# Kernel tuning notes

Measured on AMD Instinct MI355X. Metric: run time of the kernel, lower is better.

The kernel has to match this reference:

```python
import jax, jax.numpy as jnp
import numpy as np

B, S, D, H = 2, 2048, 1024, 16
HD = D // H


def setup_inputs() -> dict:
    key = jax.random.key(0)
    ks = jax.random.split(key, 9)
    sc = 0.02
    return {
        "x": jax.random.normal(ks[0], (B, S, D), dtype=jnp.float32),
        "qw": jax.random.normal(ks[1], (D, D), dtype=jnp.float32) * sc,
        "qb": jax.random.normal(ks[2], (D,), dtype=jnp.float32) * sc,
        "kw": jax.random.normal(ks[3], (D, D), dtype=jnp.float32) * sc,
        "kb": jax.random.normal(ks[4], (D,), dtype=jnp.float32) * sc,
        "vw": jax.random.normal(ks[5], (D, D), dtype=jnp.float32) * sc,
        "vb": jax.random.normal(ks[6], (D,), dtype=jnp.float32) * sc,
        "ow": jax.random.normal(ks[7], (D, D), dtype=jnp.float32) * sc,
        "ob": jax.random.normal(ks[8], (D,), dtype=jnp.float32) * sc,
    }


def reference(x, qw, qb, kw, kb, vw, vb, ow, ob):
    b, s, d = x.shape
    # projections (torch Linear: x @ W.T + b)
    q = (x @ qw.T + qb).reshape(b, s, H, HD).transpose(0, 2, 1, 3)  # bhsd
    k = (x @ kw.T + kb).reshape(b, s, H, HD).transpose(0, 2, 1, 3)
    v = (x @ vw.T + vb).reshape(b, s, H, HD).transpose(0, 2, 1, 3)
    scale = 1.0 / jnp.sqrt(jnp.float32(HD))
    score = jnp.einsum("bhsd,bhtd->bhst", q, k) * scale  # bhss
    # causal mask: -inf strictly above diagonal
    mask = jnp.triu(jnp.full((s, s), -jnp.inf, dtype=score.dtype), k=1)
    score = jax.nn.softmax(score + mask, axis=-1)
    o = jnp.einsum("bhst,bhtd->bhsd", score, v)
    o = o.transpose(0, 2, 1, 3).reshape(b, s, d)
    return o @ ow.T + ob
```

## Files before the change

kernel.cpp:

```cpp
#include <hip/hip_runtime.h>
#include <hip/hip_bf16.h>
#include <stdint.h>

typedef __bf16 bf16x8 __attribute__((ext_vector_type(8)));
typedef __bf16 bf16x4 __attribute__((ext_vector_type(4)));
typedef float f32x4 __attribute__((ext_vector_type(4)));
typedef unsigned short ushort_t;


__device__ inline ushort_t f2bf(float f) {
  union { float f; uint32_t u; } v; v.f = f;
  uint32_t r = (v.u + 0x7fffu + ((v.u >> 16) & 1u)) >> 16;
  return (ushort_t)r;
}

__device__ inline void gll16(const void* g, void* l) {
  __builtin_amdgcn_global_load_lds((const __attribute__((address_space(1))) void*)g,
                                   (__attribute__((address_space(3))) void*)l, 16, 0, 0);
}

__global__ void cvt_x(const float* __restrict__ in, ushort_t* __restrict__ out) {
  int i = blockIdx.x * blockDim.x + threadIdx.x;
  float4 f = ((const float4*)in)[i];
  union { ushort_t u[4]; uint2 v; } r;
  r.u[0] = f2bf(f.x); r.u[1] = f2bf(f.y); r.u[2] = f2bf(f.z); r.u[3] = f2bf(f.w);
  ((uint2*)out)[i] = r.v;
}
__global__ void cvt_w(const float* __restrict__ a, const float* __restrict__ b,
                      const float* __restrict__ c, const float* __restrict__ d,
                      ushort_t* __restrict__ out) {
  const float* srcs[4] = {a, b, c, d};
  const float* s = srcs[blockIdx.y];
  ushort_t* o = out + (size_t)blockIdx.y * 1048576;
  int i = blockIdx.x * blockDim.x + threadIdx.x;
  float4 f = ((const float4*)s)[i];
  union { ushort_t u[4]; uint2 v; } r;
  r.u[0] = f2bf(f.x); r.u[1] = f2bf(f.y); r.u[2] = f2bf(f.z); r.u[3] = f2bf(f.w);
  ((uint2*)(o))[i] = r.v;
}

__global__ __launch_bounds__(256) void qkv_gemm(
    const ushort_t* __restrict__ xb,
    const ushort_t* __restrict__ qwb, const ushort_t* __restrict__ kwb, const ushort_t* __restrict__ vwb,
    const float* __restrict__ qbias, const float* __restrict__ kbias, const float* __restrict__ vbias,
    ushort_t* __restrict__ qo, ushort_t* __restrict__ ko, ushort_t* __restrict__ vto)
{
  const int z = blockIdx.z;
  const float* bias = (z == 0) ? qbias : (z == 1) ? kbias : vbias;
  const ushort_t* Ap;
  const ushort_t* Bp;
  int m0, n0;
  if (z == 2) {
    Ap = vwb; Bp = xb;
    m0 = blockIdx.x * 128;
    n0 = blockIdx.y * 128;
  } else {
    Ap = xb; Bp = (z == 0) ? qwb : kwb;
    m0 = blockIdx.y * 128;
    n0 = blockIdx.x * 128;
  }

  __shared__ __align__(16) ushort_t As[128 * 64];
  __shared__ __align__(16) ushort_t Bs[128 * 64];

  const int tid = threadIdx.x;
  const int w = tid >> 6;
  const int lane = tid & 63;
  const int ln = lane & 15;
  const int q4 = lane >> 4;
  const int wm = w & 1, wn = w >> 1;

  f32x4 acc[4][4];
  #pragma unroll
  for (int i = 0; i < 4; i++)
    #pragma unroll
    for (int j = 0; j < 4; j++) acc[i][j] = f32x4{0.f, 0.f, 0.f, 0.f};

  for (int k0 = 0; k0 < 1024; k0 += 64) {
    __syncthreads();
    #pragma unroll
    for (int i = 0; i < 4; i++) {
      int c = tid + i * 256;
      int row = c >> 3;
      int cq = (c & 7) ^ (row & 7);
      gll16(&Ap[(size_t)(m0 + row) * 1024 + k0 + cq * 8], &As[c * 8]);
      gll16(&Bp[(size_t)(n0 + row) * 1024 + k0 + cq * 8], &Bs[c * 8]);
    }
    __syncthreads();
    #pragma unroll
    for (int ks = 0; ks < 2; ks++) {
      bf16x8 af[4], bfr[4];
      #pragma unroll
      for (int t = 0; t < 4; t++) {
        int rr = wm * 64 + t * 16 + ln;
        af[t]  = *(const bf16x8*)(&As[rr * 64 + (((ks * 4 + q4) ^ (rr & 7)) * 8)]);
        int rc = wn * 64 + t * 16 + ln;
        bfr[t] = *(const bf16x8*)(&Bs[rc * 64 + (((ks * 4 + q4) ^ (rc & 7)) * 8)]);
      }
      #pragma unroll
      for (int tm = 0; tm < 4; tm++)
        #pragma unroll
        for (int tn = 0; tn < 4; tn++)
          acc[tm][tn] = __builtin_amdgcn_mfma_f32_16x16x32_bf16(af[tm], bfr[tn], acc[tm][tn], 0, 0, 0);
    }
  }

  if (z == 2) {
    #pragma unroll
    for (int tn = 0; tn < 4; tn++) {
      int col = n0 + wn * 64 + tn * 16 + ln;
      int bb = col >> 11, s = col & 2047;
      size_t base = (size_t)bb * 2097152 + s;
      #pragma unroll
      for (int tm = 0; tm < 4; tm++) {
        int prow = m0 + wm * 64 + tm * 16 + q4 * 4;
        #pragma unroll
        for (int r = 0; r < 4; r++) {
          int p = prow + r;
          vto[base + (size_t)p * 2048] = f2bf(acc[tm][tn][r] + bias[p]);
        }
      }
    }
  } else {
    #pragma unroll
    for (int tn = 0; tn < 4; tn++) {
      int col = n0 + wn * 64 + tn * 16 + ln;
      float bv = bias[col];
      int h = col >> 6, hd = col & 63;
      #pragma unroll
      for (int tm = 0; tm < 4; tm++) {
        int rowb = m0 + wm * 64 + tm * 16 + q4 * 4;
        #pragma unroll
        for (int r = 0; r < 4; r++) {
          int row = rowb + r;
          int b = row >> 11, s = row & 2047;
          float val = acc[tm][tn][r] + bv;
          if (z == 0) {
            qo[((size_t)((b * 16 + h) * 2048 + s)) * 64 + hd] = f2bf(val * 0.180336884f);
          } else {
            ko[((size_t)((b * 16 + h) * 2048 + s)) * 64 + hd] = f2bf(val);
          }
        }
      }
    }
  }
}

#define PAD 72
#define PPAD 68
__global__ __launch_bounds__(256) void attn(
    const ushort_t* __restrict__ qp, const ushort_t* __restrict__ kp,
    const ushort_t* __restrict__ vtp, ushort_t* __restrict__ op)
{
  __shared__ __align__(16) ushort_t Ks[64 * PAD];
  __shared__ __align__(16) ushort_t Vts[64 * PAD];
  __shared__ __align__(16) ushort_t Ps[8][16 * PPAD];

  const int tid = threadIdx.x;
  const int w = tid >> 6;
  const int lane = tid & 63;
  const int ln = lane & 15;
  const int q4 = lane >> 4;
  const int bh = blockIdx.y;
  const int b = bh >> 4, h = bh & 15;
  int tswz = (blockIdx.x + blockIdx.y) & 15;
  const int qt = (blockIdx.y & 16) ? (15 - tswz) : tswz;
  const int q0 = qt * 128;
  const int nt = 2 * qt + 2;

  const int c0 = tid, c1 = tid + 256;
  const int kr0_row = c0 >> 3, kr0_col = (c0 & 7) * 8;
  const int kr1_row = c1 >> 3, kr1_col = (c1 & 7) * 8;

  bf16x8 onesf;
  {
    union { ushort_t u[8]; bf16x8 v; } t;
    #pragma unroll
    for (int j = 0; j < 8; j++) t.u[j] = 0x3F80;
    onesf = t.v;
  }

  bf16x8 qf[2][2];
  #pragma unroll
  for (int s = 0; s < 2; s++) {
    const ushort_t* base = qp + ((size_t)bh * 2048 + q0 + w * 32 + s * 16 + ln) * 64 + q4 * 8;
    qf[s][0] = *(const bf16x8*)(base);
    qf[s][1] = *(const bf16x8*)(base + 32);
  }

  f32x4 acc_o[2][4];
  f32x4 acc_l[2];
  #pragma unroll
  for (int s = 0; s < 2; s++) {
    acc_l[s] = f32x4{0.f, 0.f, 0.f, 0.f};
    #pragma unroll
    for (int t = 0; t < 4; t++) acc_o[s][t] = f32x4{0.f, 0.f, 0.f, 0.f};
  }

  uint4 kr0, kr1, vr0, vr1;
  {
    const ushort_t* kb = kp + (size_t)bh * 2048 * 64;
    kr0 = *(const uint4*)(kb + kr0_row * 64 + kr0_col);
    kr1 = *(const uint4*)(kb + kr1_row * 64 + kr1_col);
    const ushort_t* vb = vtp + (size_t)bh * 64 * 2048;
    vr0 = *(const uint4*)(vb + (size_t)kr0_row * 2048 + kr0_col);
    vr1 = *(const uint4*)(vb + (size_t)kr1_row * 2048 + kr1_col);
  }

  for (int it = 0; it < nt; it++) {
    if (it) __syncthreads();
    *(uint4*)(&Ks [kr0_row * PAD + kr0_col]) = kr0;
    *(uint4*)(&Ks [kr1_row * PAD + kr1_col]) = kr1;
    *(uint4*)(&Vts[kr0_row * PAD + kr0_col]) = vr0;
    *(uint4*)(&Vts[kr1_row * PAD + kr1_col]) = vr1;
    __syncthreads();

    if (it + 1 < nt) {
      int kv1 = (it + 1) * 64;
      const ushort_t* kb = kp + ((size_t)bh * 2048 + kv1) * 64;
      kr0 = *(const uint4*)(kb + kr0_row * 64 + kr0_col);
      kr1 = *(const uint4*)(kb + kr1_row * 64 + kr1_col);
      const ushort_t* vb = vtp + (size_t)bh * 64 * 2048;
      vr0 = *(const uint4*)(vb + (size_t)kr0_row * 2048 + kv1 + kr0_col);
      vr1 = *(const uint4*)(vb + (size_t)kr1_row * 2048 + kv1 + kr1_col);
    }

    f32x4 sc[2][4];
    #pragma unroll
    for (int s = 0; s < 2; s++)
      #pragma unroll
      for (int t = 0; t < 4; t++) sc[s][t] = f32x4{0.f, 0.f, 0.f, 0.f};
    #pragma unroll
    for (int ks = 0; ks < 2; ks++) {
      bf16x8 kf[4];
      #pragma unroll
      for (int tn = 0; tn < 4; tn++)
        kf[tn] = *(const bf16x8*)(&Ks[(tn * 16 + ln) * PAD + ks * 32 + q4 * 8]);
      #pragma unroll
      for (int s = 0; s < 2; s++)
        #pragma unroll
        for (int tn = 0; tn < 4; tn++)
          sc[s][tn] = __builtin_amdgcn_mfma_f32_16x16x32_bf16(qf[s][ks], kf[tn], sc[s][tn], 0, 0, 0);
    }
    if (it >= 2 * qt) {
      int kv0 = it * 64;
      #pragma unroll
      for (int s = 0; s < 2; s++) {
        int qrow = q0 + w * 32 + s * 16 + q4 * 4;
        #pragma unroll
        for (int tn = 0; tn < 4; tn++) {
          int col = kv0 + tn * 16 + ln;
          #pragma unroll
          for (int r = 0; r < 4; r++)
            if (col > qrow + r) sc[s][tn][r] = -__builtin_inff();
        }
      }
    }
    #pragma unroll
    for (int s = 0; s < 2; s++)
      #pragma unroll
      for (int tn = 0; tn < 4; tn++)
        #pragma unroll
        for (int r = 0; r < 4; r++) {
          float p = __builtin_amdgcn_exp2f(sc[s][tn][r]);
          Ps[w * 2 + s][(q4 * 4 + r) * PPAD + tn * 16 + ln] = (ushort_t)(__float_as_uint(p) >> 16);
        }
    #pragma unroll
    for (int ks = 0; ks < 2; ks++) {
      bf16x8 vf[4];
      #pragma unroll
      for (int tn = 0; tn < 4; tn++)
        vf[tn] = *(const bf16x8*)(&Vts[(tn * 16 + ln) * PAD + ks * 32 + q4 * 8]);
      #pragma unroll
      for (int s = 0; s < 2; s++) {
        const ushort_t* pp = &Ps[w * 2 + s][ln * PPAD + ks * 32 + q4 * 8];
        bf16x4 plo = *(const bf16x4*)(pp);
        bf16x4 phi = *(const bf16x4*)(pp + 4);
        bf16x8 pf = __builtin_shufflevector(plo, phi, 0, 1, 2, 3, 4, 5, 6, 7);
        acc_l[s] = __builtin_amdgcn_mfma_f32_16x16x32_bf16(pf, onesf, acc_l[s], 0, 0, 0);
        #pragma unroll
        for (int tn = 0; tn < 4; tn++)
          acc_o[s][tn] = __builtin_amdgcn_mfma_f32_16x16x32_bf16(pf, vf[tn], acc_o[s][tn], 0, 0, 0);
      }
    }
  }

  #pragma unroll
  for (int s = 0; s < 2; s++) {
    float invl[4];
    #pragma unroll
    for (int r = 0; r < 4; r++) invl[r] = __builtin_amdgcn_rcpf(acc_l[s][r]);
    #pragma unroll
    for (int tn = 0; tn < 4; tn++)
      #pragma unroll
      for (int r = 0; r < 4; r++) {
        int row = q0 + w * 32 + s * 16 + q4 * 4 + r;
        op[((size_t)b * 2048 + row) * 1024 + h * 64 + tn * 16 + ln] =
            f2bf(acc_o[s][tn][r] * invl[r]);
      }
  }
}

__global__ __launch_bounds__(256) void out_gemm(
    const ushort_t* __restrict__ ob_in, const ushort_t* __restrict__ owb,
    const float* __restrict__ obias, float* __restrict__ out)
{
  __shared__ __align__(16) ushort_t As[64 * 64];
  __shared__ __align__(16) ushort_t Bs[128 * 64];

  const int tid = threadIdx.x;
  const int w = tid >> 6;
  const int lane = tid & 63;
  const int ln = lane & 15;
  const int q4 = lane >> 4;
  const int wm = w & 1, wn = w >> 1;
  const int m0 = blockIdx.y * 64;
  const int n0 = blockIdx.x * 128;

  f32x4 acc[2][4];
  #pragma unroll
  for (int i = 0; i < 2; i++)
    #pragma unroll
    for (int j = 0; j < 4; j++) acc[i][j] = f32x4{0.f, 0.f, 0.f, 0.f};

  for (int k0 = 0; k0 < 1024; k0 += 64) {
    __syncthreads();
    #pragma unroll
    for (int i = 0; i < 2; i++) {
      int c = tid + i * 256;
      int row = c >> 3;
      int cq = (c & 7) ^ (row & 7);
      gll16(&ob_in[(size_t)(m0 + row) * 1024 + k0 + cq * 8], &As[c * 8]);
    }
    #pragma unroll
    for (int i = 0; i < 4; i++) {
      int c = tid + i * 256;
      int row = c >> 3;
      int cq = (c & 7) ^ (row & 7);
      gll16(&owb[(size_t)(n0 + row) * 1024 + k0 + cq * 8], &Bs[c * 8]);
    }
    __syncthreads();
    #pragma unroll
    for (int ks = 0; ks < 2; ks++) {
      bf16x8 af[2], bfr[4];
      #pragma unroll
      for (int t = 0; t < 2; t++) {
        int rr = wm * 32 + t * 16 + ln;
        af[t] = *(const bf16x8*)(&As[rr * 64 + (((ks * 4 + q4) ^ (rr & 7)) * 8)]);
      }
      #pragma unroll
      for (int t = 0; t < 4; t++) {
        int rc = wn * 64 + t * 16 + ln;
        bfr[t] = *(const bf16x8*)(&Bs[rc * 64 + (((ks * 4 + q4) ^ (rc & 7)) * 8)]);
      }
      #pragma unroll
      for (int tm = 0; tm < 2; tm++)
        #pragma unroll
        for (int tn = 0; tn < 4; tn++)
          acc[tm][tn] = __builtin_amdgcn_mfma_f32_16x16x32_bf16(af[tm], bfr[tn], acc[tm][tn], 0, 0, 0);
    }
  }

  #pragma unroll
  for (int tn = 0; tn < 4; tn++) {
    int col = n0 + wn * 64 + tn * 16 + ln;
    float bv = obias[col];
    #pragma unroll
    for (int tm = 0; tm < 2; tm++) {
      int rowb = m0 + wm * 32 + tm * 16 + q4 * 4;
      #pragma unroll
      for (int r = 0; r < 4; r++)
        out[(size_t)(rowb + r) * 1024 + col] = acc[tm][tn][r] + bv;
    }
  }
}

extern "C" void kernel_launch(void* const* d_in, const int* in_sizes, int n_in,
                              void* d_out, int out_size, void* d_ws, size_t ws_size,
                              hipStream_t stream) {
  const float* x     = (const float*)d_in[0];
  const float* qw    = (const float*)d_in[1];
  const float* qb    = (const float*)d_in[2];
  const float* kw    = (const float*)d_in[3];
  const float* kb    = (const float*)d_in[4];
  const float* vw    = (const float*)d_in[5];
  const float* vb    = (const float*)d_in[6];
  const float* ow    = (const float*)d_in[7];
  const float* obias = (const float*)d_in[8];
  float* out = (float*)d_out;

  char* ws = (char*)d_ws;
  ushort_t* xb  = (ushort_t*)(ws);
  ushort_t* wb  = (ushort_t*)(ws + 8388608);
  ushort_t* qwb = wb;
  ushort_t* kwb = wb + 1048576;
  ushort_t* vwb = wb + 2097152;
  ushort_t* owb = wb + 3145728;
  ushort_t* qo  = (ushort_t*)(ws + 16777216);
  ushort_t* ko  = (ushort_t*)(ws + 25165824);
  ushort_t* vto = (ushort_t*)(ws + 33554432);
  ushort_t* oo  = (ushort_t*)(ws + 41943040);

  cvt_x<<<dim3(4096), dim3(256), 0, stream>>>(x, xb);
  cvt_w<<<dim3(1024, 4), dim3(256), 0, stream>>>(qw, kw, vw, ow, wb);

  qkv_gemm<<<dim3(8, 32, 3), dim3(256), 0, stream>>>(xb, qwb, kwb, vwb, qb, kb, vb, qo, ko, vto);
  attn<<<dim3(16, 32), dim3(256), 0, stream>>>(qo, ko, vto, oo);
  out_gemm<<<dim3(8, 64), dim3(256), 0, stream>>>(oo, owb, obias, out);
}
```

Before: 191.7 us.

## Rewrite QKV GEMM as 256x256-tile, 8-wave, double-buffered pipelined kernel

The QKV projection GEMM moves from 128x128 tiles with 4 waves and a single LDS buffer to 256x256 tiles with 8 waves. Global-to-LDS loads are double-buffered and interleaved with four MFMA phases per k-step, using explicit barriers, waitcnt and s_setprio. The aim is to hide load latency behind compute and raise reuse per tile. The cost is that the grid shrinks to 192 blocks, which may underfill the 256 CUs, and the large LDS and register footprint limits occupancy.

```diff
diff --git a/kernel.cpp b/kernel.cpp
--- a/kernel.cpp
+++ b/kernel.cpp
@@ -39,102 +39,192 @@
   ((uint2*)(o))[i] = r.v;
 }
 
-__global__ __launch_bounds__(256) void qkv_gemm(
+#define NKT 16
+
+__device__ inline void stage_half(const ushort_t* __restrict__ g, ushort_t* l, int tid) {
+  #pragma unroll
+  for (int i = 0; i < 2; i++) {
+    int c = tid + i * 512;
+    int row = c >> 3;
+    int q = (c & 7) ^ (row & 7);
+    gll16(g + (size_t)row * 1024 + q * 8, l + c * 8);
+  }
+}
+
+__global__ __launch_bounds__(512, 2) void qkv_gemm(
     const ushort_t* __restrict__ xb,
     const ushort_t* __restrict__ qwb, const ushort_t* __restrict__ kwb, const ushort_t* __restrict__ vwb,
     const float* __restrict__ qbias, const float* __restrict__ kbias, const float* __restrict__ vbias,
     ushort_t* __restrict__ qo, ushort_t* __restrict__ ko, ushort_t* __restrict__ vto)
 {
-  const int z = blockIdx.z;
+  const int z = blockIdx.y;
+  const int bx = blockIdx.x;
   const float* bias = (z == 0) ? qbias : (z == 1) ? kbias : vbias;
   const ushort_t* Ap;
   const ushort_t* Bp;
   int m0, n0;
   if (z == 2) {
     Ap = vwb; Bp = xb;
-    m0 = blockIdx.x * 128;
-    n0 = blockIdx.y * 128;
+    m0 = (bx & 3) * 256;
+    n0 = (bx >> 2) * 256;
   } else {
     Ap = xb; Bp = (z == 0) ? qwb : kwb;
-    m0 = blockIdx.y * 128;
-    n0 = blockIdx.x * 128;
-  }
-
-  __shared__ __align__(16) ushort_t As[128 * 64];
-  __shared__ __align__(16) ushort_t Bs[128 * 64];
+    m0 = (bx >> 2) * 256;
+    n0 = (bx & 3) * 256;
+  }
+
+  __shared__ __align__(16) ushort_t As[2][2][128 * 64];
+  __shared__ __align__(16) ushort_t Bs[2][2][128 * 64];
 
   const int tid = threadIdx.x;
   const int w = tid >> 6;
   const int lane = tid & 63;
   const int ln = lane & 15;
   const int q4 = lane >> 4;
-  const int wm = w & 1, wn = w >> 1;
-
-  f32x4 acc[4][4];
-  #pragma unroll
-  for (int i = 0; i < 4; i++)
+  const int wm = w & 1;
+  const int wn = w >> 1;
+  const int bh = wn >> 1;
+  const int brow0 = (wn & 1) * 64;
+
+  f32x4 acc[8][4];
+  #pragma unroll
+  for (int i = 0; i < 8; i++)
     #pragma unroll
     for (int j = 0; j < 4; j++) acc[i][j] = f32x4{0.f, 0.f, 0.f, 0.f};
 
-  for (int k0 = 0; k0 < 1024; k0 += 64) {
-    __syncthreads();
-    #pragma unroll
-    for (int i = 0; i < 4; i++) {
-      int c = tid + i * 256;
-      int row = c >> 3;
-      int cq = (c & 7) ^ (row & 7);
-      gll16(&Ap[(size_t)(m0 + row) * 1024 + k0 + cq * 8], &As[c * 8]);
-      gll16(&Bp[(size_t)(n0 + row) * 1024 + k0 + cq * 8], &Bs[c * 8]);
-    }
-    __syncthreads();
-    #pragma unroll
-    for (int ks = 0; ks < 2; ks++) {
-      bf16x8 af[4], bfr[4];
-      #pragma unroll
-      for (int t = 0; t < 4; t++) {
-        int rr = wm * 64 + t * 16 + ln;
-        af[t]  = *(const bf16x8*)(&As[rr * 64 + (((ks * 4 + q4) ^ (rr & 7)) * 8)]);
-        int rc = wn * 64 + t * 16 + ln;
-        bfr[t] = *(const bf16x8*)(&Bs[rc * 64 + (((ks * 4 + q4) ^ (rc & 7)) * 8)]);
-      }
-      #pragma unroll
-      for (int tm = 0; tm < 4; tm++)
-        #pragma unroll
-        for (int tn = 0; tn < 4; tn++)
-          acc[tm][tn] = __builtin_amdgcn_mfma_f32_16x16x32_bf16(af[tm], bfr[tn], acc[tm][tn], 0, 0, 0);
-    }
+  stage_half(Ap + (size_t)(m0 +   0) * 1024 +  0, &As[0][0][0], tid);
+  stage_half(Ap + (size_t)(m0 + 128) * 1024 +  0, &As[0][1][0], tid);
+  stage_half(Bp + (size_t)(n0 +   0) * 1024 +  0, &Bs[0][0][0], tid);
+  stage_half(Bp + (size_t)(n0 + 128) * 1024 +  0, &Bs[0][1][0], tid);
+  stage_half(Bp + (size_t)(n0 +   0) * 1024 + 64, &Bs[1][0][0], tid);
+  stage_half(Bp + (size_t)(n0 + 128) * 1024 + 64, &Bs[1][1][0], tid);
+  asm volatile("s_waitcnt vmcnt(4)" ::: "memory");
+  __builtin_amdgcn_s_barrier();
+
+  const int achk = ln & 7;
+
+  for (int t = 0; t < NKT; ++t) {
+    const int buf = t & 1;
+    const ushort_t* Abuf = &As[buf][wm][0];
+    const ushort_t* Bbuf = &Bs[buf][bh][0];
+
+    bf16x8 a0[4][2], a4[4][2], b0[2][2], b2[2][2];
+
+    #pragma unroll
+    for (int m = 0; m < 4; m++)
+      #pragma unroll
+      for (int ks = 0; ks < 2; ks++)
+        a0[m][ks] = *(const bf16x8*)&Abuf[(m * 16 + ln) * 64 + (((ks * 4 + q4) ^ achk) * 8)];
+    #pragma unroll
+    for (int n = 0; n < 2; n++)
+      #pragma unroll
+      for (int ks = 0; ks < 2; ks++)
+        b0[n][ks] = *(const bf16x8*)&Bbuf[(brow0 + n * 16 + ln) * 64 + (((ks * 4 + q4) ^ achk) * 8)];
+    if (t + 1 < NKT)
+      stage_half(Ap + (size_t)m0 * 1024 + (t + 1) * 64, &As[(t + 1) & 1][0][0], tid);
+    __builtin_amdgcn_s_barrier();
+    asm volatile("s_waitcnt lgkmcnt(0)" ::: "memory");
+    __builtin_amdgcn_s_setprio(1);
+    #pragma unroll
+    for (int m = 0; m < 4; m++)
+      #pragma unroll
+      for (int n = 0; n < 2; n++)
+        #pragma unroll
+        for (int ks = 0; ks < 2; ks++)
+          acc[m][n] = __builtin_amdgcn_mfma_f32_16x16x32_bf16(a0[m][ks], b0[n][ks], acc[m][n], 0, 0, 0);
+    __builtin_amdgcn_s_setprio(0);
+    __builtin_amdgcn_s_barrier();
+
+    #pragma unroll
+    for (int n = 0; n < 2; n++)
+      #pragma unroll
+      for (int ks = 0; ks < 2; ks++)
+        b2[n][ks] = *(const bf16x8*)&Bbuf[(brow0 + (n + 2) * 16 + ln) * 64 + (((ks * 4 + q4) ^ achk) * 8)];
+    if (t + 1 < NKT)
+      stage_half(Ap + (size_t)(m0 + 128) * 1024 + (t + 1) * 64, &As[(t + 1) & 1][1][0], tid);
+    __builtin_amdgcn_s_barrier();
+    asm volatile("s_waitcnt lgkmcnt(0)" ::: "memory");
+    __builtin_amdgcn_s_setprio(1);
+    #pragma unroll
+    for (int m = 0; m < 4; m++)
+      #pragma unroll
+      for (int n = 0; n < 2; n++)
+        #pragma unroll
+        for (int ks = 0; ks < 2; ks++)
+          acc[m][n + 2] = __builtin_amdgcn_mfma_f32_16x16x32_bf16(a0[m][ks], b2[n][ks], acc[m][n + 2], 0, 0, 0);
+    __builtin_amdgcn_s_setprio(0);
+    __builtin_amdgcn_s_barrier();
+
+    #pragma unroll
+    for (int m = 0; m < 4; m++)
+      #pragma unroll
+      for (int ks = 0; ks < 2; ks++)
+        a4[m][ks] = *(const bf16x8*)&Abuf[((m + 4) * 16 + ln) * 64 + (((ks * 4 + q4) ^ achk) * 8)];
+    if (t + 2 < NKT)
+      stage_half(Bp + (size_t)n0 * 1024 + (t + 2) * 64, &Bs[buf][0][0], tid);
+    __builtin_amdgcn_s_barrier();
+    asm volatile("s_waitcnt lgkmcnt(0)" ::: "memory");
+    __builtin_amdgcn_s_setprio(1);
+    #pragma unroll
+    for (int m = 0; m < 4; m++)
+      #pragma unroll
+      for (int n = 0; n < 2; n++)
+        #pragma unroll
+        for (int ks = 0; ks < 2; ks++)
+          acc[m + 4][n + 2] = __builtin_amdgcn_mfma_f32_16x16x32_bf16(a4[m][ks], b2[n][ks], acc[m + 4][n + 2], 0, 0, 0);
+    __builtin_amdgcn_s_setprio(0);
+    __builtin_amdgcn_s_barrier();
+
+    if (t + 2 < NKT)
+      stage_half(Bp + (size_t)(n0 + 128) * 1024 + (t + 2) * 64, &Bs[buf][1][0], tid);
+    __builtin_amdgcn_s_barrier();
+    __builtin_amdgcn_s_setprio(1);
+    #pragma unroll
+    for (int m = 0; m < 4; m++)
+      #pragma unroll
+      for (int n = 0; n < 2; n++)
+        #pragma unroll
+        for (int ks = 0; ks < 2; ks++)
+          acc[m + 4][n] = __builtin_amdgcn_mfma_f32_16x16x32_bf16(a4[m][ks], b0[n][ks], acc[m + 4][n], 0, 0, 0);
+    __builtin_amdgcn_s_setprio(0);
+    if (t + 2 < NKT) {
+      asm volatile("s_waitcnt vmcnt(4)" ::: "memory");
+    } else if (t + 1 < NKT) {
+      asm volatile("s_waitcnt vmcnt(0)" ::: "memory");
+    }
+    __builtin_amdgcn_s_barrier();
   }
 
   if (z == 2) {
     #pragma unroll
-    for (int tn = 0; tn < 4; tn++) {
-      int col = n0 + wn * 64 + tn * 16 + ln;
+    for (int n = 0; n < 4; n++) {
+      int col = n0 + wn * 64 + n * 16 + ln;
       int bb = col >> 11, s = col & 2047;
       size_t base = (size_t)bb * 2097152 + s;
       #pragma unroll
-      for (int tm = 0; tm < 4; tm++) {
-        int prow = m0 + wm * 64 + tm * 16 + q4 * 4;
+      for (int m = 0; m < 8; m++) {
+        int prow = m0 + wm * 128 + m * 16 + q4 * 4;
         #pragma unroll
         for (int r = 0; r < 4; r++) {
           int p = prow + r;
-          vto[base + (size_t)p * 2048] = f2bf(acc[tm][tn][r] + bias[p]);
+          vto[base + (size_t)p * 2048] = f2bf(acc[m][n][r] + bias[p]);
         }
       }
     }
   } else {
     #pragma unroll
-    for (int tn = 0; tn < 4; tn++) {
-      int col = n0 + wn * 64 + tn * 16 + ln;
+    for (int n = 0; n < 4; n++) {
+      int col = n0 + wn * 64 + n * 16 + ln;
       float bv = bias[col];
       int h = col >> 6, hd = col & 63;
       #pragma unroll
-      for (int tm = 0; tm < 4; tm++) {
-        int rowb = m0 + wm * 64 + tm * 16 + q4 * 4;
+      for (int m = 0; m < 8; m++) {
+        int rowb = m0 + wm * 128 + m * 16 + q4 * 4;
         #pragma unroll
         for (int r = 0; r < 4; r++) {
           int row = rowb + r;
           int b = row >> 11, s = row & 2047;
-          float val = acc[tm][tn][r] + bv;
+          float val = acc[m][n][r] + bv;
           if (z == 0) {
             qo[((size_t)((b * 16 + h) * 2048 + s)) * 64 + hd] = f2bf(val * 0.180336884f);
           } else {
@@ -404,7 +494,7 @@
   cvt_x<<<dim3(4096), dim3(256), 0, stream>>>(x, xb);
   cvt_w<<<dim3(1024, 4), dim3(256), 0, stream>>>(qw, kw, vw, ow, wb);
 
-  qkv_gemm<<<dim3(8, 32, 3), dim3(256), 0, stream>>>(xb, qwb, kwb, vwb, qb, kb, vb, qo, ko, vto);
+  qkv_gemm<<<dim3(64, 3), dim3(512), 0, stream>>>(xb, qwb, kwb, vwb, qb, kb, vb, qo, ko, vto);
   attn<<<dim3(16, 32), dim3(256), 0, stream>>>(qo, ko, vto, oo);
   out_gemm<<<dim3(8, 64), dim3(256), 0, stream>>>(oo, owb, obias, out);
 }
```

New measurement: 184.9 us. 1.04x faster.
